# Kernel optimization log

Hardware: AMD Instinct MI355X
Metric: run time of the kernel (lower is better)

## Reference

```python
import jax, jax.numpy as jnp
import numpy as np

N_NODES = 50000
N_EDGES = 1600000
E_DIM = 128
N_LAYERS = 3
N_GRAPHS = 32


def setup_inputs() -> dict:
    key = jax.random.key(0)
    ks = jax.random.split(key, 12)
    x = jax.random.normal(ks[0], (N_NODES,), dtype=jnp.float32)
    edge_index = jax.random.randint(ks[1], (2, N_EDGES), 0, N_NODES, dtype=jnp.int32)
    batch = jnp.sort(jax.random.randint(ks[2], (N_NODES,), 0, N_GRAPHS, dtype=jnp.int32))
    s_in = 1.0  # fan_in = 1 for the first linear
    s_e = 1.0 / np.sqrt(E_DIM)
    lin_w = jax.random.normal(ks[3], (1, E_DIM), jnp.float32) * s_in
    lin_b = jax.random.normal(ks[4], (E_DIM,), jnp.float32) * 0.01
    gcn_w = jax.random.normal(ks[5], (N_LAYERS, E_DIM, E_DIM), jnp.float32) * s_e
    gcn_b = jax.random.normal(ks[6], (N_LAYERS, E_DIM), jnp.float32) * 0.01
    r1_w = jax.random.normal(ks[7], (E_DIM, E_DIM), jnp.float32) * s_e
    r1_b = jax.random.normal(ks[8], (E_DIM,), jnp.float32) * 0.01
    r2_w = jax.random.normal(ks[9], (E_DIM, 1), jnp.float32) * s_e
    r2_b = jax.random.normal(ks[10], (1,), jnp.float32) * 0.01
    return {"x": x, "edge_index": edge_index, "batch": batch,
            "lin_w": lin_w, "lin_b": lin_b, "gcn_w": gcn_w, "gcn_b": gcn_b,
            "r1_w": r1_w, "r1_b": r1_b, "r2_w": r2_w, "r2_b": r2_b}


def reference(x, edge_index, batch, lin_w, lin_b, gcn_w, gcn_b, r1_w, r1_b, r2_w, r2_b):
    # input embedding: x.view(-1, 1) @ W + b -> [N, E]
    h = x.reshape(-1, 1) @ lin_w + lin_b

    # GCN normalization (add self-loops, symmetric deg^-1/2 norm) — structure is
    # identical across layers, so compute once.
    loops = jnp.arange(N_NODES, dtype=edge_index.dtype)
    src = jnp.concatenate([edge_index[0], loops])
    dst = jnp.concatenate([edge_index[1], loops])
    deg = jax.ops.segment_sum(jnp.ones(src.shape[0], h.dtype), dst, num_segments=N_NODES)
    dinv = jnp.where(deg > 0, jax.lax.rsqrt(deg), 0.0)
    norm = (dinv[src] * dinv[dst])[:, None]  # [E+N, 1]

    # NOTE: original calls x.relu() without assignment -> no activation (faithful).
    for l in range(N_LAYERS):
        h = h @ gcn_w[l]                                        # [N, E]
        h = jax.ops.segment_sum(h[src] * norm, dst, num_segments=N_NODES) + gcn_b[l]

    # global_add_pool over graphs
    pooled = jax.ops.segment_sum(h, batch, num_segments=N_GRAPHS)  # [G, E]
    hr = jnp.tanh(pooled @ r1_w + r1_b)
    return hr @ r2_w + r2_b  # [G, 1]
```

## Files before the change

kernel.cpp:

```cpp
#include <hip/hip_runtime.h>
#include <hip/hip_bf16.h>
#include <math.h>

#define NGRAPH 32
#define CAP 10240
#define EPT 24
#define EPB (256 * EPT)

__global__ void k_part(const int* __restrict__ src, const int* __restrict__ dst,
                       int* __restrict__ gcursor, unsigned int* __restrict__ packed, int E) {
    __shared__ unsigned int ldsbuf[EPB];
    __shared__ int hist[256], lofs[256], lcur[256], base[256];
    int tid = threadIdx.x;
    int e0 = blockIdx.x * EPB;
    hist[tid] = 0;
    __syncthreads();
    int d[EPT], s[EPT];
#pragma unroll
    for (int c = 0; c < EPT / 4; c++) {
        int e = e0 + c * 1024 + (tid << 2);
        if (e + 3 < E) {
            int4 dv = *(const int4*)&dst[e];
            int4 sv = *(const int4*)&src[e];
            d[4*c+0] = dv.x; d[4*c+1] = dv.y; d[4*c+2] = dv.z; d[4*c+3] = dv.w;
            s[4*c+0] = sv.x; s[4*c+1] = sv.y; s[4*c+2] = sv.z; s[4*c+3] = sv.w;
            atomicAdd(&hist[dv.x >> 8], 1);
            atomicAdd(&hist[dv.y >> 8], 1);
            atomicAdd(&hist[dv.z >> 8], 1);
            atomicAdd(&hist[dv.w >> 8], 1);
        } else {
#pragma unroll
            for (int k = 0; k < 4; k++) {
                int ee = e + k;
                if (ee < E) {
                    d[4*c+k] = dst[ee]; s[4*c+k] = src[ee];
                    atomicAdd(&hist[d[4*c+k] >> 8], 1);
                } else {
                    d[4*c+k] = -1;
                }
            }
        }
    }
    __syncthreads();
    int v = hist[tid];
    lofs[tid] = v;
    __syncthreads();
    for (int off = 1; off < 256; off <<= 1) {
        int t = (tid >= off) ? lofs[tid - off] : 0;
        __syncthreads();
        lofs[tid] += t;
        __syncthreads();
    }
    int total = lofs[255];
    int excl = lofs[tid] - v;
    lofs[tid] = excl;
    lcur[tid] = excl;
    if (v > 0) base[tid] = tid * CAP + atomicAdd(&gcursor[tid], v);
    __syncthreads();
#pragma unroll
    for (int c = 0; c < EPT; c++) {
        int dd = d[c];
        if (dd >= 0) {
            int bk = dd >> 8;
            int slot = atomicAdd(&lcur[bk], 1);
            ldsbuf[slot] = ((unsigned int)bk << 24) | ((unsigned int)s[c] << 8)
                         | (unsigned int)(dd & 255);
        }
    }
    __syncthreads();
    for (int i = tid; i < total; i += 256) {
        unsigned int w = ldsbuf[i];
        int bk = w >> 24;
        packed[base[bk] + (i - lofs[bk])] = w & 0xFFFFFFu;
    }
}

__global__ void k_bucket(const unsigned int* __restrict__ packed, const int* __restrict__ gcursor,
                         const float* __restrict__ x, const int* __restrict__ batch,
                         int* __restrict__ offs, int* __restrict__ deg,
                         float* __restrict__ dinv, float2* __restrict__ q0,
                         unsigned short* __restrict__ csr, float* __restrict__ S, int N) {
    __shared__ int cnt[256], lofs[256], lcur[256];
    __shared__ float cs[NGRAPH];
    int tid = threadIdx.x;
    int b = blockIdx.x;
    int start = b * CAP;
    int end = start + gcursor[b];
    cnt[tid] = 0;
    if (tid < NGRAPH) cs[tid] = 0.f;
    __syncthreads();
    for (int e = start + tid; e < end; e += 256)
        atomicAdd(&cnt[packed[e] & 255], 1);
    __syncthreads();
    int v = cnt[tid];
    lofs[tid] = v;
    __syncthreads();
    for (int off = 1; off < 256; off <<= 1) {
        int t = (tid >= off) ? lofs[tid - off] : 0;
        __syncthreads();
        lofs[tid] += t;
        __syncthreads();
    }
    int excl = lofs[tid] - v;
    lcur[tid] = excl;
    int node = b * 256 + tid;
    if (node < N) {
        deg[node] = v;
        offs[node] = start + excl;
        float dv = rsqrtf((float)(v + 1));
        dinv[node] = dv;
        q0[node] = make_float2(x[node] * dv, dv);
        atomicAdd(&cs[batch[node]], 1.f);
    }
    __syncthreads();
    for (int e = start + tid; e < end; e += 256) {
        unsigned int p = packed[e];
        int pos = start + atomicAdd(&lcur[p & 255], 1);
        csr[pos] = (unsigned short)(p >> 8);
    }
    if (tid < NGRAPH && cs[tid] != 0.f) atomicAdd(&S[tid], cs[tid]);
}

template <int WRITE_Q>
__global__ void k_hop(const float2* __restrict__ qin, float2* __restrict__ pout,
                      float2* __restrict__ qout, const unsigned short* __restrict__ csr,
                      const int* __restrict__ offs, const int* __restrict__ deg,
                      const float* __restrict__ dinv, int N) {
    int tid = threadIdx.x;
    int lane = tid & 15;
    int node = blockIdx.x * 16 + (tid >> 4);
    if (node >= N) return;
    int e = offs[node], ne = deg[node];
    float sx = 0.0f, su = 0.0f;
    int j = lane;
    for (; j + 16 < ne; j += 32) {
        int i0 = csr[e + j];
        int i1 = csr[e + j + 16];
        float2 a = qin[i0];
        float2 b = qin[i1];
        sx += a.x + b.x;
        su += a.y + b.y;
    }
    if (j < ne) {
        float2 a = qin[csr[e + j]];
        sx += a.x; su += a.y;
    }
#pragma unroll
    for (int m = 8; m > 0; m >>= 1) {
        sx += __shfl_xor(sx, m);
        su += __shfl_xor(su, m);
    }
    if (lane == 0) {
        float2 qs = qin[node];
        float dv = dinv[node];
        float px = dv * (sx + qs.x), pu = dv * (su + qs.y);
        pout[node] = make_float2(px, pu);
        if (WRITE_Q) qout[node] = make_float2(px * dv, pu * dv);
    }
}

__global__ void k_sums(const float2* __restrict__ p1, const float2* __restrict__ p2,
                       const float2* __restrict__ p3, const int* __restrict__ batch,
                       float* __restrict__ S, int N) {
    __shared__ float bins[4 * NGRAPH];
    int tid = threadIdx.x;
    if (tid < 4 * NGRAPH) bins[tid] = 0.f;
    __syncthreads();
    int i = blockIdx.x * 256 + tid;
    if (i < N) {
        int g = batch[i];
        atomicAdd(&bins[g], p1[i].y);
        atomicAdd(&bins[32 + g], p2[i].y);
        atomicAdd(&bins[64 + g], p3[i].y);
        atomicAdd(&bins[96 + g], p3[i].x);
    }
    __syncthreads();
    if (tid < 4 * NGRAPH && bins[tid] != 0.f) atomicAdd(&S[32 + tid], bins[tid]);
}

__global__ void k_mlp(const float* __restrict__ S,
                      const float* __restrict__ lin_w, const float* __restrict__ lin_b,
                      const float* __restrict__ gcn_w, const float* __restrict__ gcn_b,
                      const float* __restrict__ r1_w, const float* __restrict__ r1_b,
                      const float* __restrict__ r2_w, const float* __restrict__ r2_b,
                      float* __restrict__ out) {
    __shared__ float va[128], vb[128], vc[128], vd[128], pl[128], red[128];
    int j = threadIdx.x;
    int g = blockIdx.x;
    va[j] = lin_w[j];
    vb[j] = lin_b[j];
    vc[j] = gcn_b[j];
    vd[j] = gcn_b[128 + j];
    __syncthreads();
    for (int l = 0; l < 3; l++) {
        const float* W = gcn_w + l * 128 * 128;
        float na = 0.f, nb = 0.f, nc = 0.f, nd = 0.f;
        for (int k = 0; k < 128; k++) {
            float w = W[k * 128 + j];
            na += va[k] * w;
            nb += vb[k] * w;
            nc += vc[k] * w;
            nd += vd[k] * w;
        }
        __syncthreads();
        va[j] = na; vb[j] = nb;
        if (l >= 1) vc[j] = nc;
        if (l >= 2) vd[j] = nd;
        __syncthreads();
    }
    float cnt = S[g], su1 = S[32 + g], su2 = S[64 + g], su3 = S[96 + g], sv3 = S[128 + g];
    const float* b3 = gcn_b + 2 * 128;
    pl[j] = sv3 * va[j] + su3 * vb[j] + su2 * vc[j] + su1 * vd[j] + cnt * b3[j];
    __syncthreads();
    float acc = r1_b[j];
#pragma unroll 4
    for (int k = 0; k < 128; k++) acc += pl[k] * r1_w[k * 128 + j];
    red[j] = tanhf(acc) * r2_w[j];
    __syncthreads();
    for (int sft = 64; sft > 0; sft >>= 1) {
        if (j < sft) red[j] += red[j + sft];
        __syncthreads();
    }
    if (j == 0) out[g] = red[0] + r2_b[0];
}

extern "C" void kernel_launch(void* const* d_in, const int* in_sizes, int n_in,
                              void* d_out, int out_size, void* d_ws, size_t ws_size,
                              hipStream_t stream) {
    const float* x     = (const float*)d_in[0];
    const int*   eidx  = (const int*)d_in[1];
    const int*   batch = (const int*)d_in[2];
    const float* lin_w = (const float*)d_in[3];
    const float* lin_b = (const float*)d_in[4];
    const float* gcn_w = (const float*)d_in[5];
    const float* gcn_b = (const float*)d_in[6];
    const float* r1_w  = (const float*)d_in[7];
    const float* r1_b  = (const float*)d_in[8];
    const float* r2_w  = (const float*)d_in[9];
    const float* r2_b  = (const float*)d_in[10];

    const int N = in_sizes[0];
    const int E = in_sizes[1] / 2;
    const int* src = eidx;
    const int* dst = eidx + E;
    const int NB = (N + 255) / 256;

    char* w = (char*)d_ws;
    float2* q0      = (float2*)w; w += (size_t)N * 8;
    float2* q1      = (float2*)w; w += (size_t)N * 8;
    float2* q2      = (float2*)w; w += (size_t)N * 8;
    float2* p1      = (float2*)w; w += (size_t)N * 8;
    float2* p2      = (float2*)w; w += (size_t)N * 8;
    float2* p3      = (float2*)w; w += (size_t)N * 8;
    unsigned int* packed = (unsigned int*)w; w += (size_t)256 * CAP * 4;
    int*    offs    = (int*)w;    w += (size_t)N * 4;
    int*    deg     = (int*)w;    w += (size_t)N * 4;
    float*  dinv    = (float*)w;  w += (size_t)N * 4;
    int*    gcursor = (int*)w;    w += 256 * 4;
    float*  S       = (float*)w;  w += 160 * 4;
    unsigned short* csr = (unsigned short*)w; w += (size_t)256 * CAP * 2;

    hipMemsetAsync(gcursor, 0, 256 * 4 + 160 * 4, stream);

    k_part<<<(E + EPB - 1) / EPB, 256, 0, stream>>>(src, dst, gcursor, packed, E);
    k_bucket<<<NB, 256, 0, stream>>>(packed, gcursor, x, batch, offs, deg, dinv, q0, csr, S, N);

    int hop_blocks = (N + 15) / 16;
    k_hop<1><<<hop_blocks, 256, 0, stream>>>(q0, p1, q1, csr, offs, deg, dinv, N);
    k_hop<1><<<hop_blocks, 256, 0, stream>>>(q1, p2, q2, csr, offs, deg, dinv, N);
    k_hop<0><<<hop_blocks, 256, 0, stream>>>(q2, p3, (float2*)nullptr, csr, offs, deg, dinv, N);

    k_sums<<<NB, 256, 0, stream>>>(p1, p2, p3, batch, S, N);
    k_mlp<<<NGRAPH, 128, 0, stream>>>(S, lin_w, lin_b, gcn_w, gcn_b,
                                      r1_w, r1_b, r2_w, r2_b, (float*)d_out);
}
```

Before: 173.2 us.

## Fuse pooling sums into MLP kernel and vectorize CSR index loads

The separate k_sums kernel and the p1/p2 buffers are removed. The MLP kernel now reduces each graph's contiguous node range directly, relying on the sorted batch array and per-graph counts, and recovers p from q by dividing by dinv. CSR segments are padded to even lengths so the hop kernel can load index pairs as ushort2, halving index load instructions. This saves a kernel launch and several global writes, but it moves a serial per-graph reduction into only 32 blocks and adds a division per node.

```diff
diff --git a/kernel.cpp b/kernel.cpp
--- a/kernel.cpp
+++ b/kernel.cpp
@@ -93,7 +93,8 @@
         atomicAdd(&cnt[packed[e] & 255], 1);
     __syncthreads();
     int v = cnt[tid];
-    lofs[tid] = v;
+    int vp = (v + 1) & ~1;
+    lofs[tid] = vp;
     __syncthreads();
     for (int off = 1; off < 256; off <<= 1) {
         int t = (tid >= off) ? lofs[tid - off] : 0;
@@ -101,7 +102,7 @@
         lofs[tid] += t;
         __syncthreads();
     }
-    int excl = lofs[tid] - v;
+    int excl = lofs[tid] - vp;
     lcur[tid] = excl;
     int node = b * 256 + tid;
     if (node < N) {
@@ -122,8 +123,8 @@
 }
 
 template <int WRITE_Q>
-__global__ void k_hop(const float2* __restrict__ qin, float2* __restrict__ pout,
-                      float2* __restrict__ qout, const unsigned short* __restrict__ csr,
+__global__ void k_hop(const float2* __restrict__ qin, float2* __restrict__ outv,
+                      const unsigned short* __restrict__ csr,
                       const int* __restrict__ offs, const int* __restrict__ deg,
                       const float* __restrict__ dinv, int N) {
     int tid = threadIdx.x;
@@ -132,18 +133,14 @@
     if (node >= N) return;
     int e = offs[node], ne = deg[node];
     float sx = 0.0f, su = 0.0f;
-    int j = lane;
-    for (; j + 16 < ne; j += 32) {
-        int i0 = csr[e + j];
-        int i1 = csr[e + j + 16];
-        float2 a = qin[i0];
-        float2 b = qin[i1];
-        sx += a.x + b.x;
-        su += a.y + b.y;
-    }
-    if (j < ne) {
-        float2 a = qin[csr[e + j]];
+    for (int j = 2 * lane; j < ne; j += 32) {
+        ushort2 c = *(const ushort2*)&csr[e + j];
+        float2 a = qin[c.x];
         sx += a.x; su += a.y;
+        if (j + 1 < ne) {
+            float2 b = qin[c.y];
+            sx += b.x; su += b.y;
+        }
     }
 #pragma unroll
     for (int m = 8; m > 0; m >>= 1) {
@@ -154,39 +151,50 @@
         float2 qs = qin[node];
         float dv = dinv[node];
         float px = dv * (sx + qs.x), pu = dv * (su + qs.y);
-        pout[node] = make_float2(px, pu);
-        if (WRITE_Q) qout[node] = make_float2(px * dv, pu * dv);
-    }
-}
-
-__global__ void k_sums(const float2* __restrict__ p1, const float2* __restrict__ p2,
-                       const float2* __restrict__ p3, const int* __restrict__ batch,
-                       float* __restrict__ S, int N) {
-    __shared__ float bins[4 * NGRAPH];
-    int tid = threadIdx.x;
-    if (tid < 4 * NGRAPH) bins[tid] = 0.f;
-    __syncthreads();
-    int i = blockIdx.x * 256 + tid;
-    if (i < N) {
-        int g = batch[i];
-        atomicAdd(&bins[g], p1[i].y);
-        atomicAdd(&bins[32 + g], p2[i].y);
-        atomicAdd(&bins[64 + g], p3[i].y);
-        atomicAdd(&bins[96 + g], p3[i].x);
-    }
-    __syncthreads();
-    if (tid < 4 * NGRAPH && bins[tid] != 0.f) atomicAdd(&S[32 + tid], bins[tid]);
+        if (WRITE_Q) outv[node] = make_float2(px * dv, pu * dv);
+        else         outv[node] = make_float2(px, pu);
+    }
 }
 
 __global__ void k_mlp(const float* __restrict__ S,
+                      const float2* __restrict__ q1, const float2* __restrict__ q2,
+                      const float2* __restrict__ p3, const float* __restrict__ dinv,
                       const float* __restrict__ lin_w, const float* __restrict__ lin_b,
                       const float* __restrict__ gcn_w, const float* __restrict__ gcn_b,
                       const float* __restrict__ r1_w, const float* __restrict__ r1_b,
                       const float* __restrict__ r2_w, const float* __restrict__ r2_b,
-                      float* __restrict__ out) {
+                      float* __restrict__ out, int N) {
     __shared__ float va[128], vb[128], vc[128], vd[128], pl[128], red[128];
+    __shared__ float cnts[NGRAPH];
+    __shared__ float r4[4 * 128];
     int j = threadIdx.x;
     int g = blockIdx.x;
+    if (j < NGRAPH) cnts[j] = S[j];
+    __syncthreads();
+    int r0 = 0;
+    for (int i = 0; i < g; i++) r0 += (int)cnts[i];
+    int cnt = (int)cnts[g];
+    int r1 = r0 + cnt;
+    float su1 = 0.f, su2 = 0.f, su3 = 0.f, sv3 = 0.f;
+    for (int n = r0 + j; n < r1; n += 128) {
+        float inv = 1.0f / dinv[n];
+        su1 += q1[n].y * inv;
+        su2 += q2[n].y * inv;
+        float2 p = p3[n];
+        su3 += p.y; sv3 += p.x;
+    }
+    r4[j] = su1; r4[128 + j] = su2; r4[256 + j] = su3; r4[384 + j] = sv3;
+    __syncthreads();
+    for (int sft = 64; sft > 0; sft >>= 1) {
+        if (j < sft) {
+            r4[j] += r4[j + sft];
+            r4[128 + j] += r4[128 + j + sft];
+            r4[256 + j] += r4[256 + j + sft];
+            r4[384 + j] += r4[384 + j + sft];
+        }
+        __syncthreads();
+    }
+    su1 = r4[0]; su2 = r4[128]; su3 = r4[256]; sv3 = r4[384];
     va[j] = lin_w[j];
     vb[j] = lin_b[j];
     vc[j] = gcn_b[j];
@@ -208,9 +216,8 @@
         if (l >= 2) vd[j] = nd;
         __syncthreads();
     }
-    float cnt = S[g], su1 = S[32 + g], su2 = S[64 + g], su3 = S[96 + g], sv3 = S[128 + g];
     const float* b3 = gcn_b + 2 * 128;
-    pl[j] = sv3 * va[j] + su3 * vb[j] + su2 * vc[j] + su1 * vd[j] + cnt * b3[j];
+    pl[j] = sv3 * va[j] + su3 * vb[j] + su2 * vc[j] + su1 * vd[j] + (float)cnt * b3[j];
     __syncthreads();
     float acc = r1_b[j];
 #pragma unroll 4
@@ -249,28 +256,25 @@
     float2* q0      = (float2*)w; w += (size_t)N * 8;
     float2* q1      = (float2*)w; w += (size_t)N * 8;
     float2* q2      = (float2*)w; w += (size_t)N * 8;
-    float2* p1      = (float2*)w; w += (size_t)N * 8;
-    float2* p2      = (float2*)w; w += (size_t)N * 8;
     float2* p3      = (float2*)w; w += (size_t)N * 8;
     unsigned int* packed = (unsigned int*)w; w += (size_t)256 * CAP * 4;
     int*    offs    = (int*)w;    w += (size_t)N * 4;
     int*    deg     = (int*)w;    w += (size_t)N * 4;
     float*  dinv    = (float*)w;  w += (size_t)N * 4;
     int*    gcursor = (int*)w;    w += 256 * 4;
-    float*  S       = (float*)w;  w += 160 * 4;
-    unsigned short* csr = (unsigned short*)w; w += (size_t)256 * CAP * 2;
-
-    hipMemsetAsync(gcursor, 0, 256 * 4 + 160 * 4, stream);
+    float*  S       = (float*)w;  w += 64 * 4;
+    unsigned short* csr = (unsigned short*)w; w += (size_t)256 * CAP * 2 + 256;
+
+    hipMemsetAsync(gcursor, 0, 256 * 4 + 64 * 4, stream);
 
     k_part<<<(E + EPB - 1) / EPB, 256, 0, stream>>>(src, dst, gcursor, packed, E);
     k_bucket<<<NB, 256, 0, stream>>>(packed, gcursor, x, batch, offs, deg, dinv, q0, csr, S, N);
 
     int hop_blocks = (N + 15) / 16;
-    k_hop<1><<<hop_blocks, 256, 0, stream>>>(q0, p1, q1, csr, offs, deg, dinv, N);
-    k_hop<1><<<hop_blocks, 256, 0, stream>>>(q1, p2, q2, csr, offs, deg, dinv, N);
-    k_hop<0><<<hop_blocks, 256, 0, stream>>>(q2, p3, (float2*)nullptr, csr, offs, deg, dinv, N);
-
-    k_sums<<<NB, 256, 0, stream>>>(p1, p2, p3, batch, S, N);
-    k_mlp<<<NGRAPH, 128, 0, stream>>>(S, lin_w, lin_b, gcn_w, gcn_b,
-                                      r1_w, r1_b, r2_w, r2_b, (float*)d_out);
-}
+    k_hop<1><<<hop_blocks, 256, 0, stream>>>(q0, q1, csr, offs, deg, dinv, N);
+    k_hop<1><<<hop_blocks, 256, 0, stream>>>(q1, q2, csr, offs, deg, dinv, N);
+    k_hop<0><<<hop_blocks, 256, 0, stream>>>(q2, p3, csr, offs, deg, dinv, N);
+
+    k_mlp<<<NGRAPH, 128, 0, stream>>>(S, q1, q2, p3, dinv, lin_w, lin_b, gcn_w, gcn_b,
+                                      r1_w, r1_b, r2_w, r2_b, (float*)d_out, N);
+}
```

New measurement: 177.0 us. 2.2% more time.
